# Kernel optimization log

Hardware: AMD Instinct MI355X
Metric: run time of the kernel (lower is better)

The kernel has to match this reference:

```python
import jax, jax.numpy as jnp
import numpy as np

D_PAIR = 128
NUM_HEADS = 4
LN_EPS = 1e-5


def _mha(x, w_in, b_in, w_out, b_out, num_heads):
    # x: [B, R, S, D]; attention over axis S (keys) for each query position.
    B, R, S, D = x.shape
    hd = D // num_heads
    qkv = jnp.einsum('brsd,ed->brse', x, w_in) + b_in  # [B,R,S,3D]
    q, k, v = jnp.split(qkv, 3, axis=-1)
    q = q.reshape(B, R, S, num_heads, hd)
    k = k.reshape(B, R, S, num_heads, hd)
    v = v.reshape(B, R, S, num_heads, hd)
    scores = jnp.einsum('brqhd,brkhd->brhqk', q, k) / jnp.sqrt(jnp.asarray(hd, x.dtype))
    attn = jax.nn.softmax(scores, axis=-1)
    out = jnp.einsum('brhqk,brkhd->brqhd', attn, v).reshape(B, R, S, D)
    return jnp.einsum('brsd,ed->brse', out, w_out) + b_out


def _layernorm(x, gamma, beta):
    mu = jnp.mean(x, axis=-1, keepdims=True)
    var = jnp.mean(jnp.square(x - mu), axis=-1, keepdims=True)
    return (x - mu) * jax.lax.rsqrt(var + LN_EPS) * gamma + beta


def setup_inputs() -> dict:
    key = jax.random.key(0)
    ks = jax.random.split(key, 12)
    B, L, D = 1, 256, D_PAIR
    s = 0.02
    return {
        'pair_repr': jax.random.normal(ks[0], (B, L, L, D), dtype=jnp.float32),
        'chain_id_tensor': jax.random.randint(ks[1], (L,), 0, 2),
        'w_in_s': jax.random.normal(ks[2], (3 * D, D), dtype=jnp.float32) * s,
        'b_in_s': jnp.zeros((3 * D,), jnp.float32),
        'w_out_s': jax.random.normal(ks[3], (D, D), dtype=jnp.float32) * s,
        'b_out_s': jnp.zeros((D,), jnp.float32),
        'w_in_e': jax.random.normal(ks[4], (3 * D, D), dtype=jnp.float32) * s,
        'b_in_e': jnp.zeros((3 * D,), jnp.float32),
        'w_out_e': jax.random.normal(ks[5], (D, D), dtype=jnp.float32) * s,
        'b_out_e': jnp.zeros((D,), jnp.float32),
        'gamma_s': jnp.ones((D,), jnp.float32),
        'beta_s': jnp.zeros((D,), jnp.float32),
        'gamma_e': jnp.ones((D,), jnp.float32),
        'beta_e': jnp.zeros((D,), jnp.float32),
        'w_gate': jax.random.normal(ks[6], (D, D), dtype=jnp.float32) * s,
        'b_gate': jnp.zeros((D,), jnp.float32),
    }


def reference(pair_repr, chain_id_tensor, w_in_s, b_in_s, w_out_s, b_out_s,
              w_in_e, b_in_e, w_out_e, b_out_e, gamma_s, beta_s,
              gamma_e, beta_e, w_gate, b_gate):
    # Row-wise (starting node) attention: attend over axis 2.
    attn_i = _mha(pair_repr, w_in_s, b_in_s, w_out_s, b_out_s, NUM_HEADS)
    pair = _layernorm(pair_repr + attn_i, gamma_s, beta_s)
    # Column-wise (ending node) attention: transpose rows/cols, attend, transpose back.
    pair_t = jnp.swapaxes(pair, 1, 2)
    attn_j = _mha(pair_t, w_in_e, b_in_e, w_out_e, b_out_e, NUM_HEADS)
    pair = _layernorm(pair + jnp.swapaxes(attn_j, 1, 2), gamma_e, beta_e)
    gate = jax.nn.sigmoid(jnp.einsum('bijd,ed->bije', pair, w_gate) + b_gate)
    return pair * gate
```

## Files before the change

### kernel.cpp

```cpp
#include <hip/hip_runtime.h>
#include <hip/hip_bf16.h>
#include <cstddef>

#define DD 128

typedef unsigned short u16;
typedef short short8v __attribute__((ext_vector_type(8)));
typedef float floatx4 __attribute__((ext_vector_type(4)));

__device__ __forceinline__ float bf2f(u16 u) {
    return __uint_as_float(((unsigned int)u) << 16);
}
__device__ __forceinline__ u16 f2b(float x) {
    unsigned u = __float_as_uint(x);
    return (u16)((u + 0x7FFF + ((u >> 16) & 1)) >> 16);
}
__device__ __forceinline__ unsigned cvtpk_bf16(float lo, float hi) {
    unsigned r;
    asm("v_cvt_pk_bf16_f32 %0, %1, %2" : "=v"(r) : "v"(lo), "v"(hi));
    return r;
}

__device__ __forceinline__ void stage_w_bf16(const float* __restrict__ Wf,
                                             u16* __restrict__ Wl, int tid) {
    #pragma unroll
    for (int it = 0; it < 8; ++it) {
        int f = tid + it * 512;
        int row = f >> 5, c4 = f & 31;
        float4 v = reinterpret_cast<const float4*>(Wf + (size_t)row * DD)[c4];
        ushort4 o;
        o.x = f2b(v.x); o.y = f2b(v.y); o.z = f2b(v.z); o.w = f2b(v.w);
        *reinterpret_cast<ushort4*>(&Wl[row * 136 + c4 * 4]) = o;
    }
}

__global__ __launch_bounds__(512) void proj_qkv_mfma(
    const float* __restrict__ X, const float* __restrict__ Wf,
    const float* __restrict__ bias, __hip_bfloat16* __restrict__ QKo,
    __hip_bfloat16* __restrict__ VTo, int transposed)
{
    __shared__ u16 Wl[128 * 136];
    const int tid = threadIdx.x;
    const int tok0 = blockIdx.x * 128;
    const int lane = tid & 63, wq = tid >> 6;
    const int lq = lane & 15, g = lane >> 4;
    const int t = tok0 + wq * 16 + lq;
    const int xrow = transposed ? ((t & 255) * 256 + (t >> 8)) : t;

    short8v bfrag[4];
    #pragma unroll
    for (int ks = 0; ks < 4; ++ks) {
        const float* p = X + (size_t)xrow * DD + ks * 32 + g * 8;
        float4 a = *reinterpret_cast<const float4*>(p);
        float4 b = *reinterpret_cast<const float4*>(p + 4);
        u16 tmp[8] = { f2b(a.x), f2b(a.y), f2b(a.z), f2b(a.w),
                       f2b(b.x), f2b(b.y), f2b(b.z), f2b(b.w) };
        bfrag[ks] = *reinterpret_cast<const short8v*>(tmp);
    }

    u16* qkt = reinterpret_cast<u16*>(QKo) + (size_t)t * 256;
    u16* vtb = reinterpret_cast<u16*>(VTo);
    const int rr_ = t >> 8, kk_ = t & 255;

    for (int c = 0; c < 3; ++c) {
        if (c) __syncthreads();
        stage_w_bf16(Wf + (size_t)c * 128 * DD, Wl, tid);
        __syncthreads();
        #pragma unroll
        for (int et = 0; et < 8; ++et) {
            float4 b4 = *reinterpret_cast<const float4*>(bias + c * 128 + et * 16 + g * 4);
            floatx4 acc = { b4.x, b4.y, b4.z, b4.w };
            #pragma unroll
            for (int ks = 0; ks < 4; ++ks) {
                short8v afrag = *reinterpret_cast<const short8v*>(
                    &Wl[(et * 16 + lq) * 136 + ks * 32 + g * 8]);
                acc = __builtin_amdgcn_mfma_f32_16x16x32_bf16(afrag, bfrag[ks], acc, 0, 0, 0);
            }
            if (c < 2) {
                ushort4 o;
                o.x = f2b(acc[0]); o.y = f2b(acc[1]); o.z = f2b(acc[2]); o.w = f2b(acc[3]);
                *reinterpret_cast<ushort4*>(&qkt[c * 128 + et * 16 + g * 4]) = o;
            } else {
                int e = et * 16 + g * 4;
                int hh = e >> 5, dbase = e & 31;
                u16* vb = vtb + ((size_t)(rr_ * 4 + hh) * 32 + dbase) * 256 + kk_;
                vb[0]   = f2b(acc[0]);
                vb[256] = f2b(acc[1]);
                vb[512] = f2b(acc[2]);
                vb[768] = f2b(acc[3]);
            }
        }
    }
}

__global__ __launch_bounds__(512, 6) void attn_mfma_kernel(
    const __hip_bfloat16* __restrict__ QK, const __hip_bfloat16* __restrict__ VT,
    __hip_bfloat16* __restrict__ O)
{
    constexpr int KP = 40;
    constexpr int VP = 264;
    __shared__ u16 K_lds[256 * KP];
    __shared__ u16 Vt_lds[32 * VP];

    const int tid = threadIdx.x;
    const int h = blockIdx.x, r = blockIdx.y;
    const u16* qk = reinterpret_cast<const u16*>(QK) + (size_t)r * 256 * 256;
    const u16* vt = reinterpret_cast<const u16*>(VT) + ((size_t)r * 4 + h) * 8192;

    #pragma unroll
    for (int it = 0; it < 2; ++it) {
        int f = tid + it * 512;
        int row = f >> 2, c = f & 3;
        uint4 v = *reinterpret_cast<const uint4*>(qk + (size_t)row * 256 + 128 + h * 32 + c * 8);
        *reinterpret_cast<uint4*>(&K_lds[row * KP + c * 8]) = v;
    }
    #pragma unroll
    for (int it = 0; it < 2; ++it) {
        int f = tid + it * 512;
        int row = f >> 5, c = f & 31;
        uint4 v = *reinterpret_cast<const uint4*>(vt + row * 256 + c * 8);
        *reinterpret_cast<uint4*>(&Vt_lds[row * VP + c * 8]) = v;
    }
    __syncthreads();

    const int lane = tid & 63;
    const int wq = tid >> 6;
    const int lq = lane & 15;
    const int g  = lane >> 4;
    const int bp0 = ((g & 1) * 32 + lq) * 4;
    const int bp1 = bp0 + 64;
    const bool hi_half = lane >= 32;
    const float C1 = 0.25505654196988f;

    #pragma unroll
    for (int mq = 0; mq < 2; ++mq) {
        const int q0 = wq * 32 + mq * 16;
        short8v qfrag = *reinterpret_cast<const short8v*>(
            qk + (size_t)(q0 + lq) * 256 + h * 32 + g * 8);

        floatx4 s[16];
        __builtin_amdgcn_s_setprio(1);
        #pragma unroll
        for (int ni = 0; ni < 16; ++ni) {
            short8v kfrag = *reinterpret_cast<const short8v*>(&K_lds[(ni * 16 + lq) * KP + g * 8]);
            floatx4 z = {0.f, 0.f, 0.f, 0.f};
            s[ni] = __builtin_amdgcn_mfma_f32_16x16x32_bf16(kfrag, qfrag, z, 0, 0, 0);
        }
        __builtin_amdgcn_s_setprio(0);

        float m = -1e30f;
        #pragma unroll
        for (int ni = 0; ni < 16; ++ni)
            m = fmaxf(fmaxf(fmaxf(m, s[ni][0]), fmaxf(s[ni][1], s[ni][2])), s[ni][3]);
        m = fmaxf(m, __shfl_xor(m, 16));
        m = fmaxf(m, __shfl_xor(m, 32));
        const float m1 = m * C1;

        float ell = 0.f;
        unsigned u[32];
        #pragma unroll
        for (int ni = 0; ni < 16; ++ni) {
            float p0 = __builtin_amdgcn_exp2f(__builtin_fmaf(s[ni][0], C1, -m1));
            float p1 = __builtin_amdgcn_exp2f(__builtin_fmaf(s[ni][1], C1, -m1));
            float p2 = __builtin_amdgcn_exp2f(__builtin_fmaf(s[ni][2], C1, -m1));
            float p3 = __builtin_amdgcn_exp2f(__builtin_fmaf(s[ni][3], C1, -m1));
            ell += (p0 + p1) + (p2 + p3);
            u[2 * ni]     = cvtpk_bf16(p0, p1);
            u[2 * ni + 1] = cvtpk_bf16(p2, p3);
        }
        ell += __shfl_xor(ell, 16);
        ell += __shfl_xor(ell, 32);

        floatx4 o0 = {0.f, 0.f, 0.f, 0.f}, o1 = {0.f, 0.f, 0.f, 0.f};
        __builtin_amdgcn_s_setprio(1);
        #pragma unroll
        for (int ks = 0; ks < 8; ++ks) {
            unsigned Y0 = hi_half ? u[4 * ks + 2] : u[4 * ks];
            unsigned Y1 = hi_half ? u[4 * ks + 3] : u[4 * ks + 1];
            int w0 = __builtin_amdgcn_ds_bpermute(bp0, (int)Y0);
            int w1 = __builtin_amdgcn_ds_bpermute(bp0, (int)Y1);
            int w2 = __builtin_amdgcn_ds_bpermute(bp1, (int)Y0);
            int w3 = __builtin_amdgcn_ds_bpermute(bp1, (int)Y1);
            union { int i[4]; short8v v; } pu;
            pu.i[0] = w0; pu.i[1] = w1; pu.i[2] = w2; pu.i[3] = w3;
            short8v v0 = *reinterpret_cast<const short8v*>(&Vt_lds[lq * VP + ks * 32 + g * 8]);
            short8v v1 = *reinterpret_cast<const short8v*>(&Vt_lds[(16 + lq) * VP + ks * 32 + g * 8]);
            o0 = __builtin_amdgcn_mfma_f32_16x16x32_bf16(v0, pu.v, o0, 0, 0, 0);
            o1 = __builtin_amdgcn_mfma_f32_16x16x32_bf16(v1, pu.v, o1, 0, 0, 0);
        }
        __builtin_amdgcn_s_setprio(0);

        const float inv = 1.f / ell;
        __hip_bfloat16* orow = O + ((size_t)r * 256 + q0 + lq) * 128 + h * 32;
        ushort4 w0s, w1s;
        w0s.x = f2b(o0[0] * inv); w0s.y = f2b(o0[1] * inv);
        w0s.z = f2b(o0[2] * inv); w0s.w = f2b(o0[3] * inv);
        w1s.x = f2b(o1[0] * inv); w1s.y = f2b(o1[1] * inv);
        w1s.z = f2b(o1[2] * inv); w1s.w = f2b(o1[3] * inv);
        *reinterpret_cast<ushort4*>(reinterpret_cast<u16*>(orow) + g * 4) = w0s;
        *reinterpret_cast<ushort4*>(reinterpret_cast<u16*>(orow) + 16 + g * 4) = w1s;
    }
}

__global__ __launch_bounds__(512) void proj_ln_mfma(
    const __hip_bfloat16* __restrict__ A, const float* __restrict__ Wf,
    const float* __restrict__ bias, const float* __restrict__ RES,
    const float* __restrict__ gamma, const float* __restrict__ beta,
    float* __restrict__ OUT, int transposed)
{
    __shared__ u16 Wl[128 * 136];
    const int tid = threadIdx.x;
    const int tok0 = blockIdx.x * 128;
    const int lane = tid & 63, wq = tid >> 6;
    const int lq = lane & 15, g = lane >> 4;
    const int t = tok0 + wq * 16 + lq;
    const int arow = transposed ? ((t & 255) * 256 + (t >> 8)) : t;
    const u16* A16 = reinterpret_cast<const u16*>(A);

    stage_w_bf16(Wf, Wl, tid);

    short8v bfrag[4];
    #pragma unroll
    for (int ks = 0; ks < 4; ++ks)
        bfrag[ks] = *reinterpret_cast<const short8v*>(A16 + (size_t)arow * DD + ks * 32 + g * 8);

    __syncthreads();

    floatx4 acc[8];
    #pragma unroll
    for (int et = 0; et < 8; ++et) {
        float4 b4 = *reinterpret_cast<const float4*>(bias + et * 16 + g * 4);
        float4 r4 = *reinterpret_cast<const float4*>(RES + (size_t)t * DD + et * 16 + g * 4);
        acc[et] = { b4.x + r4.x, b4.y + r4.y, b4.z + r4.z, b4.w + r4.w };
        #pragma unroll
        for (int ks = 0; ks < 4; ++ks) {
            short8v afrag = *reinterpret_cast<const short8v*>(
                &Wl[(et * 16 + lq) * 136 + ks * 32 + g * 8]);
            acc[et] = __builtin_amdgcn_mfma_f32_16x16x32_bf16(afrag, bfrag[ks], acc[et], 0, 0, 0);
        }
    }

    float s = 0.f, ss = 0.f;
    #pragma unroll
    for (int et = 0; et < 8; ++et)
        #pragma unroll
        for (int rr = 0; rr < 4; ++rr) { float v = acc[et][rr]; s += v; ss += v * v; }
    s  += __shfl_xor(s, 16);  s  += __shfl_xor(s, 32);
    ss += __shfl_xor(ss, 16); ss += __shfl_xor(ss, 32);
    float mu = s * (1.f / 128.f);
    float var = ss * (1.f / 128.f) - mu * mu;
    float rstd = rsqrtf(var + 1e-5f);

    #pragma unroll
    for (int et = 0; et < 8; ++et) {
        float4 g4 = *reinterpret_cast<const float4*>(gamma + et * 16 + g * 4);
        float4 be4 = *reinterpret_cast<const float4*>(beta + et * 16 + g * 4);
        float4 o4;
        o4.x = (acc[et][0] - mu) * rstd * g4.x + be4.x;
        o4.y = (acc[et][1] - mu) * rstd * g4.y + be4.y;
        o4.z = (acc[et][2] - mu) * rstd * g4.z + be4.z;
        o4.w = (acc[et][3] - mu) * rstd * g4.w + be4.w;
        *reinterpret_cast<float4*>(OUT + (size_t)t * DD + et * 16 + g * 4) = o4;
    }
}

__global__ __launch_bounds__(512) void proj_ln_gate_mfma(
    const __hip_bfloat16* __restrict__ A, const float* __restrict__ Wf,
    const float* __restrict__ bias, const float* __restrict__ RES,
    const float* __restrict__ gamma, const float* __restrict__ beta,
    const float* __restrict__ Wgf, const float* __restrict__ bg,
    float* __restrict__ OUT, int transposed)
{
    __shared__ u16 Wl[128 * 136];
    __shared__ u16 Yl[128 * 136];
    const int tid = threadIdx.x;
    const int tok0 = blockIdx.x * 128;
    const int lane = tid & 63, wq = tid >> 6;
    const int lq = lane & 15, g = lane >> 4;
    const int tl = wq * 16 + lq;
    const int t = tok0 + tl;
    const int arow = transposed ? ((t & 255) * 256 + (t >> 8)) : t;
    const u16* A16 = reinterpret_cast<const u16*>(A);

    stage_w_bf16(Wf, Wl, tid);

    short8v bfrag[4];
    #pragma unroll
    for (int ks = 0; ks < 4; ++ks)
        bfrag[ks] = *reinterpret_cast<const short8v*>(A16 + (size_t)arow * DD + ks * 32 + g * 8);

    __syncthreads();

    floatx4 acc[8];
    #pragma unroll
    for (int et = 0; et < 8; ++et) {
        float4 b4 = *reinterpret_cast<const float4*>(bias + et * 16 + g * 4);
        float4 r4 = *reinterpret_cast<const float4*>(RES + (size_t)t * DD + et * 16 + g * 4);
        acc[et] = { b4.x + r4.x, b4.y + r4.y, b4.z + r4.z, b4.w + r4.w };
        #pragma unroll
        for (int ks = 0; ks < 4; ++ks) {
            short8v afrag = *reinterpret_cast<const short8v*>(
                &Wl[(et * 16 + lq) * 136 + ks * 32 + g * 8]);
            acc[et] = __builtin_amdgcn_mfma_f32_16x16x32_bf16(afrag, bfrag[ks], acc[et], 0, 0, 0);
        }
    }

    float s = 0.f, ss = 0.f;
    #pragma unroll
    for (int et = 0; et < 8; ++et)
        #pragma unroll
        for (int rr = 0; rr < 4; ++rr) { float v = acc[et][rr]; s += v; ss += v * v; }
    s  += __shfl_xor(s, 16);  s  += __shfl_xor(s, 32);
    ss += __shfl_xor(ss, 16); ss += __shfl_xor(ss, 32);
    float mu = s * (1.f / 128.f);
    float var = ss * (1.f / 128.f) - mu * mu;
    float rstd = rsqrtf(var + 1e-5f);

    #pragma unroll
    for (int et = 0; et < 8; ++et) {
        float4 g4 = *reinterpret_cast<const float4*>(gamma + et * 16 + g * 4);
        float4 be4 = *reinterpret_cast<const float4*>(beta + et * 16 + g * 4);
        acc[et][0] = (acc[et][0] - mu) * rstd * g4.x + be4.x;
        acc[et][1] = (acc[et][1] - mu) * rstd * g4.y + be4.y;
        acc[et][2] = (acc[et][2] - mu) * rstd * g4.z + be4.z;
        acc[et][3] = (acc[et][3] - mu) * rstd * g4.w + be4.w;
        ushort4 yb;
        yb.x = f2b(acc[et][0]); yb.y = f2b(acc[et][1]);
        yb.z = f2b(acc[et][2]); yb.w = f2b(acc[et][3]);
        *reinterpret_cast<ushort4*>(&Yl[tl * 136 + et * 16 + g * 4]) = yb;
    }

    __syncthreads();
    stage_w_bf16(Wgf, Wl, tid);
    __syncthreads();

    short8v yfrag[4];
    #pragma unroll
    for (int ks = 0; ks < 4; ++ks)
        yfrag[ks] = *reinterpret_cast<const short8v*>(&Yl[tl * 136 + ks * 32 + g * 8]);

    #pragma unroll
    for (int et = 0; et < 8; ++et) {
        float4 b4 = *reinterpret_cast<const float4*>(bg + et * 16 + g * 4);
        floatx4 z = { b4.x, b4.y, b4.z, b4.w };
        #pragma unroll
        for (int ks = 0; ks < 4; ++ks) {
            short8v afrag = *reinterpret_cast<const short8v*>(
                &Wl[(et * 16 + lq) * 136 + ks * 32 + g * 8]);
            z = __builtin_amdgcn_mfma_f32_16x16x32_bf16(afrag, yfrag[ks], z, 0, 0, 0);
        }
        float4 o4;
        o4.x = acc[et][0] / (1.f + __expf(-z[0]));
        o4.y = acc[et][1] / (1.f + __expf(-z[1]));
        o4.z = acc[et][2] / (1.f + __expf(-z[2]));
        o4.w = acc[et][3] / (1.f + __expf(-z[3]));
        *reinterpret_cast<float4*>(OUT + (size_t)t * DD + et * 16 + g * 4) = o4;
    }
}

extern "C" void kernel_launch(void* const* d_in, const int* in_sizes, int n_in,
                              void* d_out, int out_size, void* d_ws, size_t ws_size,
                              hipStream_t stream) {
    const float* pair    = (const float*)d_in[0];
    const float* w_in_s  = (const float*)d_in[2];
    const float* b_in_s  = (const float*)d_in[3];
    const float* w_out_s = (const float*)d_in[4];
    const float* b_out_s = (const float*)d_in[5];
    const float* w_in_e  = (const float*)d_in[6];
    const float* b_in_e  = (const float*)d_in[7];
    const float* w_out_e = (const float*)d_in[8];
    const float* b_out_e = (const float*)d_in[9];
    const float* gamma_s = (const float*)d_in[10];
    const float* beta_s  = (const float*)d_in[11];
    const float* gamma_e = (const float*)d_in[12];
    const float* beta_e  = (const float*)d_in[13];
    const float* w_gate  = (const float*)d_in[14];
    const float* b_gate  = (const float*)d_in[15];
    float* out = (float*)d_out;

    __hip_bfloat16* qk   = (__hip_bfloat16*)d_ws;
    __hip_bfloat16* vt   = qk + (size_t)65536 * 256;
    __hip_bfloat16* attn = vt + (size_t)1024 * 32 * 256;

    proj_qkv_mfma<<<512, 512, 0, stream>>>(pair, w_in_s, b_in_s, qk, vt, 0);
    attn_mfma_kernel<<<dim3(4, 256), 512, 0, stream>>>(qk, vt, attn);
    proj_ln_mfma<<<512, 512, 0, stream>>>(attn, w_out_s, b_out_s, pair,
                                          gamma_s, beta_s, out, 0);
    proj_qkv_mfma<<<512, 512, 0, stream>>>(out, w_in_e, b_in_e, qk, vt, 1);
    attn_mfma_kernel<<<dim3(4, 256), 512, 0, stream>>>(qk, vt, attn);
    proj_ln_gate_mfma<<<512, 512, 0, stream>>>(attn, w_out_e, b_out_e, out,
                                               gamma_e, beta_e, w_gate, b_gate,
                                               out, 1);
}
```

Before: 141.6 us.

## Pre-convert weights to bf16 and write transposed bf16 activations for column pass

Adds a small kernel that converts all weight matrices to bf16 once, so every projection block copies ready-made bf16 weights into LDS instead of converting fp32 per block. The first layernorm kernel also writes a bf16 copy of its output in transposed token order, which the second QKV projection reads contiguously. The second attention pass scatters its output back into the original token order, so the final projection and gate kernel read rows directly. This removes strided gathers and repeated fp32-to-bf16 conversion, at the cost of an extra kernel launch, a second activation write, and scattered stores in attention.

```diff
diff --git a/kernel.cpp b/kernel.cpp
--- a/kernel.cpp
+++ b/kernel.cpp
@@ -8,9 +8,6 @@
 typedef short short8v __attribute__((ext_vector_type(8)));
 typedef float floatx4 __attribute__((ext_vector_type(4)));
 
-__device__ __forceinline__ float bf2f(u16 u) {
-    return __uint_as_float(((unsigned int)u) << 16);
-}
 __device__ __forceinline__ u16 f2b(float x) {
     unsigned u = __float_as_uint(x);
     return (u16)((u + 0x7FFF + ((u >> 16) & 1)) >> 16);
@@ -21,23 +18,39 @@
     return r;
 }
 
-__device__ __forceinline__ void stage_w_bf16(const float* __restrict__ Wf,
-                                             u16* __restrict__ Wl, int tid) {
-    #pragma unroll
-    for (int it = 0; it < 8; ++it) {
+__global__ __launch_bounds__(512) void wcvt_kernel(
+    const float* __restrict__ a0, const float* __restrict__ a1,
+    const float* __restrict__ a2, const float* __restrict__ a3,
+    const float* __restrict__ a4, u16* __restrict__ dst)
+{
+    int q = blockIdx.x * 512 + threadIdx.x;
+    int i = q * 4;
+    const float* src; int off;
+    if      (i < 49152)  { src = a0; off = 0; }
+    else if (i < 65536)  { src = a1; off = 49152; }
+    else if (i < 114688) { src = a2; off = 65536; }
+    else if (i < 131072) { src = a3; off = 114688; }
+    else                 { src = a4; off = 131072; }
+    float4 v = *reinterpret_cast<const float4*>(src + (i - off));
+    ushort4 o = { f2b(v.x), f2b(v.y), f2b(v.z), f2b(v.w) };
+    *reinterpret_cast<ushort4*>(dst + i) = o;
+}
+
+__device__ __forceinline__ void stage_wb(const u16* __restrict__ Wb,
+                                         u16* __restrict__ Wl, int tid) {
+    #pragma unroll
+    for (int it = 0; it < 4; ++it) {
         int f = tid + it * 512;
-        int row = f >> 5, c4 = f & 31;
-        float4 v = reinterpret_cast<const float4*>(Wf + (size_t)row * DD)[c4];
-        ushort4 o;
-        o.x = f2b(v.x); o.y = f2b(v.y); o.z = f2b(v.z); o.w = f2b(v.w);
-        *reinterpret_cast<ushort4*>(&Wl[row * 136 + c4 * 4]) = o;
+        int row = f >> 4, c8 = f & 15;
+        uint4 v = *reinterpret_cast<const uint4*>(Wb + (size_t)row * DD + c8 * 8);
+        *reinterpret_cast<uint4*>(&Wl[row * 136 + c8 * 8]) = v;
     }
 }
 
 __global__ __launch_bounds__(512) void proj_qkv_mfma(
-    const float* __restrict__ X, const float* __restrict__ Wf,
-    const float* __restrict__ bias, __hip_bfloat16* __restrict__ QKo,
-    __hip_bfloat16* __restrict__ VTo, int transposed)
+    const float* __restrict__ Xf, const u16* __restrict__ Xb,
+    const u16* __restrict__ Wb, const float* __restrict__ bias,
+    __hip_bfloat16* __restrict__ QKo, __hip_bfloat16* __restrict__ VTo)
 {
     __shared__ u16 Wl[128 * 136];
     const int tid = threadIdx.x;
@@ -45,17 +58,22 @@
     const int lane = tid & 63, wq = tid >> 6;
     const int lq = lane & 15, g = lane >> 4;
     const int t = tok0 + wq * 16 + lq;
-    const int xrow = transposed ? ((t & 255) * 256 + (t >> 8)) : t;
 
     short8v bfrag[4];
-    #pragma unroll
-    for (int ks = 0; ks < 4; ++ks) {
-        const float* p = X + (size_t)xrow * DD + ks * 32 + g * 8;
-        float4 a = *reinterpret_cast<const float4*>(p);
-        float4 b = *reinterpret_cast<const float4*>(p + 4);
-        u16 tmp[8] = { f2b(a.x), f2b(a.y), f2b(a.z), f2b(a.w),
-                       f2b(b.x), f2b(b.y), f2b(b.z), f2b(b.w) };
-        bfrag[ks] = *reinterpret_cast<const short8v*>(tmp);
+    if (Xb) {
+        #pragma unroll
+        for (int ks = 0; ks < 4; ++ks)
+            bfrag[ks] = *reinterpret_cast<const short8v*>(Xb + (size_t)t * DD + ks * 32 + g * 8);
+    } else {
+        #pragma unroll
+        for (int ks = 0; ks < 4; ++ks) {
+            const float* p = Xf + (size_t)t * DD + ks * 32 + g * 8;
+            float4 a = *reinterpret_cast<const float4*>(p);
+            float4 b = *reinterpret_cast<const float4*>(p + 4);
+            u16 tmp[8] = { f2b(a.x), f2b(a.y), f2b(a.z), f2b(a.w),
+                           f2b(b.x), f2b(b.y), f2b(b.z), f2b(b.w) };
+            bfrag[ks] = *reinterpret_cast<const short8v*>(tmp);
+        }
     }
 
     u16* qkt = reinterpret_cast<u16*>(QKo) + (size_t)t * 256;
@@ -64,7 +82,7 @@
 
     for (int c = 0; c < 3; ++c) {
         if (c) __syncthreads();
-        stage_w_bf16(Wf + (size_t)c * 128 * DD, Wl, tid);
+        stage_wb(Wb + (size_t)c * 128 * DD, Wl, tid);
         __syncthreads();
         #pragma unroll
         for (int et = 0; et < 8; ++et) {
@@ -95,7 +113,7 @@
 
 __global__ __launch_bounds__(512, 6) void attn_mfma_kernel(
     const __hip_bfloat16* __restrict__ QK, const __hip_bfloat16* __restrict__ VT,
-    __hip_bfloat16* __restrict__ O)
+    __hip_bfloat16* __restrict__ O, int swap_store)
 {
     constexpr int KP = 40;
     constexpr int VP = 264;
@@ -191,7 +209,9 @@
         __builtin_amdgcn_s_setprio(0);
 
         const float inv = 1.f / ell;
-        __hip_bfloat16* orow = O + ((size_t)r * 256 + q0 + lq) * 128 + h * 32;
+        const size_t opos = swap_store ? ((size_t)(q0 + lq) * 256 + r)
+                                       : ((size_t)r * 256 + q0 + lq);
+        __hip_bfloat16* orow = O + opos * 128 + h * 32;
         ushort4 w0s, w1s;
         w0s.x = f2b(o0[0] * inv); w0s.y = f2b(o0[1] * inv);
         w0s.z = f2b(o0[2] * inv); w0s.w = f2b(o0[3] * inv);
@@ -203,10 +223,10 @@
 }
 
 __global__ __launch_bounds__(512) void proj_ln_mfma(
-    const __hip_bfloat16* __restrict__ A, const float* __restrict__ Wf,
+    const __hip_bfloat16* __restrict__ A, const u16* __restrict__ Wb,
     const float* __restrict__ bias, const float* __restrict__ RES,
     const float* __restrict__ gamma, const float* __restrict__ beta,
-    float* __restrict__ OUT, int transposed)
+    float* __restrict__ OUT, u16* __restrict__ Xt)
 {
     __shared__ u16 Wl[128 * 136];
     const int tid = threadIdx.x;
@@ -214,15 +234,14 @@
     const int lane = tid & 63, wq = tid >> 6;
     const int lq = lane & 15, g = lane >> 4;
     const int t = tok0 + wq * 16 + lq;
-    const int arow = transposed ? ((t & 255) * 256 + (t >> 8)) : t;
     const u16* A16 = reinterpret_cast<const u16*>(A);
 
-    stage_w_bf16(Wf, Wl, tid);
+    stage_wb(Wb, Wl, tid);
 
     short8v bfrag[4];
     #pragma unroll
     for (int ks = 0; ks < 4; ++ks)
-        bfrag[ks] = *reinterpret_cast<const short8v*>(A16 + (size_t)arow * DD + ks * 32 + g * 8);
+        bfrag[ks] = *reinterpret_cast<const short8v*>(A16 + (size_t)t * DD + ks * 32 + g * 8);
 
     __syncthreads();
 
@@ -251,6 +270,7 @@
     float var = ss * (1.f / 128.f) - mu * mu;
     float rstd = rsqrtf(var + 1e-5f);
 
+    u16* xt = Xt + (size_t)((t & 255) * 256 + (t >> 8)) * DD;
     #pragma unroll
     for (int et = 0; et < 8; ++et) {
         float4 g4 = *reinterpret_cast<const float4*>(gamma + et * 16 + g * 4);
@@ -261,15 +281,17 @@
         o4.z = (acc[et][2] - mu) * rstd * g4.z + be4.z;
         o4.w = (acc[et][3] - mu) * rstd * g4.w + be4.w;
         *reinterpret_cast<float4*>(OUT + (size_t)t * DD + et * 16 + g * 4) = o4;
+        ushort4 xb = { f2b(o4.x), f2b(o4.y), f2b(o4.z), f2b(o4.w) };
+        *reinterpret_cast<ushort4*>(&xt[et * 16 + g * 4]) = xb;
     }
 }
 
 __global__ __launch_bounds__(512) void proj_ln_gate_mfma(
-    const __hip_bfloat16* __restrict__ A, const float* __restrict__ Wf,
+    const __hip_bfloat16* __restrict__ A, const u16* __restrict__ Wb,
     const float* __restrict__ bias, const float* __restrict__ RES,
     const float* __restrict__ gamma, const float* __restrict__ beta,
-    const float* __restrict__ Wgf, const float* __restrict__ bg,
-    float* __restrict__ OUT, int transposed)
+    const u16* __restrict__ Wgb, const float* __restrict__ bg,
+    float* __restrict__ OUT)
 {
     __shared__ u16 Wl[128 * 136];
     __shared__ u16 Yl[128 * 136];
@@ -279,15 +301,14 @@
     const int lq = lane & 15, g = lane >> 4;
     const int tl = wq * 16 + lq;
     const int t = tok0 + tl;
-    const int arow = transposed ? ((t & 255) * 256 + (t >> 8)) : t;
     const u16* A16 = reinterpret_cast<const u16*>(A);
 
-    stage_w_bf16(Wf, Wl, tid);
+    stage_wb(Wb, Wl, tid);
 
     short8v bfrag[4];
     #pragma unroll
     for (int ks = 0; ks < 4; ++ks)
-        bfrag[ks] = *reinterpret_cast<const short8v*>(A16 + (size_t)arow * DD + ks * 32 + g * 8);
+        bfrag[ks] = *reinterpret_cast<const short8v*>(A16 + (size_t)t * DD + ks * 32 + g * 8);
 
     __syncthreads();
 
@@ -331,7 +352,7 @@
     }
 
     __syncthreads();
-    stage_w_bf16(Wgf, Wl, tid);
+    stage_wb(Wgb, Wl, tid);
     __syncthreads();
 
     short8v yfrag[4];
@@ -381,14 +402,18 @@
     __hip_bfloat16* qk   = (__hip_bfloat16*)d_ws;
     __hip_bfloat16* vt   = qk + (size_t)65536 * 256;
     __hip_bfloat16* attn = vt + (size_t)1024 * 32 * 256;
-
-    proj_qkv_mfma<<<512, 512, 0, stream>>>(pair, w_in_s, b_in_s, qk, vt, 0);
-    attn_mfma_kernel<<<dim3(4, 256), 512, 0, stream>>>(qk, vt, attn);
-    proj_ln_mfma<<<512, 512, 0, stream>>>(attn, w_out_s, b_out_s, pair,
-                                          gamma_s, beta_s, out, 0);
-    proj_qkv_mfma<<<512, 512, 0, stream>>>(out, w_in_e, b_in_e, qk, vt, 1);
-    attn_mfma_kernel<<<dim3(4, 256), 512, 0, stream>>>(qk, vt, attn);
-    proj_ln_gate_mfma<<<512, 512, 0, stream>>>(attn, w_out_e, b_out_e, out,
-                                               gamma_e, beta_e, w_gate, b_gate,
-                                               out, 1);
-}
+    u16*            xt   = (u16*)(attn + (size_t)65536 * 128);
+    u16*            wb   = xt + (size_t)65536 * 128;
+
+    wcvt_kernel<<<80, 512, 0, stream>>>(w_in_s, w_out_s, w_in_e, w_out_e, w_gate, wb);
+
+    proj_qkv_mfma<<<512, 512, 0, stream>>>(pair, nullptr, wb, b_in_s, qk, vt);
+    attn_mfma_kernel<<<dim3(4, 256), 512, 0, stream>>>(qk, vt, attn, 0);
+    proj_ln_mfma<<<512, 512, 0, stream>>>(attn, wb + 49152, b_out_s, pair,
+                                          gamma_s, beta_s, out, xt);
+    proj_qkv_mfma<<<512, 512, 0, stream>>>(nullptr, xt, wb + 65536, b_in_e, qk, vt);
+    attn_mfma_kernel<<<dim3(4, 256), 512, 0, stream>>>(qk, vt, attn, 1);
+    proj_ln_gate_mfma<<<512, 512, 0, stream>>>(attn, wb + 114688, b_out_e, out,
+                                               gamma_e, beta_e, wb + 131072, b_gate,
+                                               out);
+}
```

Result: no change. 142.7 us (+0.8%).
